# Optimization experiments

Measured on AMD Instinct MI355X. Metric: run time of the kernel, lower is better.

## Reference

```python
import jax, jax.numpy as jnp
import numpy as np

TEMPERATURE = 0.07


def _l2norm(x, axis, eps=1e-12):
    n = jnp.sqrt(jnp.sum(x * x, axis=axis, keepdims=True))
    return x / jnp.maximum(n, eps)


def _bilinear_sample(img, x, y):
    # img: (C,H,W); x,y: (N,) pixel coords. Matches F.grid_sample(mode='bilinear',
    # padding_mode='zeros', align_corners=True) after the norm/denorm round trip.
    C, H, W = img.shape
    x0 = jnp.floor(x); y0 = jnp.floor(y)
    x1 = x0 + 1.0;     y1 = y0 + 1.0
    wx1 = x - x0; wx0 = 1.0 - wx1
    wy1 = y - y0; wy0 = 1.0 - wy1

    def gather(xi, yi, w):
        inb = (xi >= 0) & (xi <= W - 1) & (yi >= 0) & (yi <= H - 1)
        xc = jnp.clip(xi, 0, W - 1).astype(jnp.int32)
        yc = jnp.clip(yi, 0, H - 1).astype(jnp.int32)
        v = img[:, yc, xc]  # (C,N)
        return v * (w * inb)[None, :]

    return (gather(x0, y0, wx0 * wy0) + gather(x1, y0, wx1 * wy0)
            + gather(x0, y1, wx0 * wy1) + gather(x1, y1, wx1 * wy1))


def setup_inputs() -> dict:
    key = jax.random.key(0)
    k1, k2, k3, k4 = jax.random.split(key, 4)
    B, C, Hf, Wf = 32, 256, 64, 64
    Ho, Wo = 512, 512
    fmap_rgb = jax.random.normal(k1, (B, C, Hf, Wf), dtype=jnp.float32)
    fmap_depth = jax.random.normal(k2, (B, C, Hf, Wf), dtype=jnp.float32)
    # uniform coords inside the original image so sampled positions are in-range
    projected_coords = jax.random.uniform(k3, (B, 2, Ho, Wo), dtype=jnp.float32) * (Wo - 1)
    valid_mask = jax.random.uniform(k4, (B, 1, Ho, Wo), dtype=jnp.float32)
    return {"fmap_rgb": fmap_rgb, "fmap_depth": fmap_depth,
            "projected_coords": projected_coords, "valid_mask": valid_mask}


def reference(fmap_rgb, fmap_depth, projected_coords, valid_mask):
    B, C, Hf, Wf = fmap_rgb.shape
    Ho = projected_coords.shape[2]
    ds = Ho // Hf

    fr = _l2norm(fmap_rgb, axis=1)
    fd = _l2norm(fmap_depth, axis=1)

    coords_f = projected_coords[:, :, ::ds, ::ds]   # (B,2,Hf,Wf)
    vm_f = valid_mask[:, :, ::ds, ::ds]             # (B,1,Hf,Wf)

    step = max(1, Hf // 16)
    gh, gw = jnp.meshgrid(jnp.arange(0, Hf, step), jnp.arange(0, Wf, step), indexing='ij')
    ghf = gh.reshape(-1); gwf = gw.reshape(-1)
    N = ghf.shape[0]  # num_grid (~256)

    depth_feats = fd[:, :, ghf, gwf]                # (B,C,N)
    rgb_neg = fr[:, :, ghf, gwf]                    # (B,C,N)
    proj_u = coords_f[:, 0, ghf, gwf] / ds          # (B,N) pixel coords in feat space
    proj_v = coords_f[:, 1, ghf, gwf] / ds
    grid_valid = vm_f[:, 0, ghf, gwf] > 0.5         # (B,N)

    # positive features via bilinear sampling (computed in the original; not used
    # in the loss because labels index into rgb_neg, i.e. the diagonal)
    _rgb_pos = jax.vmap(_bilinear_sample)(fr, proj_u, proj_v)  # (B,C,N)

    sim = jnp.einsum('bcn,bcm->bnm', depth_feats, rgb_neg) / TEMPERATURE  # (B,N,N)

    neg_inf = jnp.asarray(-1e30, sim.dtype)
    sim_m = jnp.where(grid_valid[:, None, :], sim, neg_inf)  # mask invalid columns
    logZ = jax.nn.logsumexp(sim_m, axis=-1)                  # (B,N)
    diag = jnp.einsum('bnn->bn', sim)                        # positive logits
    row_loss = logZ - diag                                   # per-row CE

    vf = grid_valid.astype(sim.dtype)
    n_valid = grid_valid.sum(axis=-1)                        # (B,) int
    include = n_valid >= 2                                   # skip batches with <2 valid
    loss_b = (row_loss * vf).sum(axis=-1) / jnp.maximum(n_valid, 1).astype(sim.dtype)
    avg_loss = jnp.where(include, loss_b, 0.0).sum() / B

    preds = jnp.argmax(sim_m, axis=-1)                       # (B,N)
    correct = (preds == jnp.arange(N)[None, :]) & grid_valid & include[:, None]
    total_count = jnp.where(include, n_valid, 0).sum()
    accuracy = jnp.where(total_count > 0,
                         correct.sum().astype(sim.dtype) /
                         jnp.maximum(total_count, 1).astype(sim.dtype) * 100.0,
                         0.0)
    avg_loss = jnp.where(total_count > 0, avg_loss, 0.0)
    return avg_loss, accuracy
```

## Files before the change

### kernel.cpp

```cpp
#include <hip/hip_runtime.h>
#include <math.h>

#define BB   32
#define CC   256
#define HF   64
#define WF   64
#define NN   256
#define MROWS 32
#define NSTRIP (NN / MROWS)
#define SIMP 260
#define NXCD 8

typedef __attribute__((ext_vector_type(8))) short    bf16x8;
typedef __attribute__((ext_vector_type(4))) float    f32x4;
typedef __attribute__((ext_vector_type(8))) unsigned short u16x8;

__device__ inline unsigned short f2bf(float f) {
    unsigned u = __float_as_uint(f);
    unsigned r = u + 0x7FFFu + ((u >> 16) & 1u);
    return (unsigned short)(r >> 16);
}

__global__ __launch_bounds__(256) void gather_kernel(
        const float* __restrict__ fr,
        const float* __restrict__ fd,
        const float* __restrict__ vm,
        unsigned short* __restrict__ Dbf,
        unsigned short* __restrict__ Rbf,
        float* __restrict__ nPartD,
        float* __restrict__ nPartR,
        float* __restrict__ GV) {
    int blk = blockIdx.x;
    int xcd = blk & (NXCD - 1);
    int r   = blk >> 3;
    int b   = xcd * 4 + (r & 3);
    int cg  = r >> 2;

    int t = threadIdx.x;
    int i = t >> 4, j = t & 15;

    size_t mapBase = (size_t)(b * CC + cg * 16) * (HF * WF);
    size_t ptOff   = (size_t)(4 * i) * WF + 4 * j;

    float ssd = 0.0f, ssr = 0.0f;
    unsigned short dbuf[16], rbuf[16];
#pragma unroll
    for (int cc = 0; cc < 16; ++cc) {
        float vd_ = fd[mapBase + (size_t)cc * (HF * WF) + ptOff];
        float vr_ = fr[mapBase + (size_t)cc * (HF * WF) + ptOff];
        dbuf[cc] = f2bf(vd_);
        rbuf[cc] = f2bf(vr_);
        ssd = fmaf(vd_, vd_, ssd);
        ssr = fmaf(vr_, vr_, ssr);
    }
    unsigned short* dDst = Dbf + ((size_t)(b * NN + t) * CC + cg * 16);
    unsigned short* rDst = Rbf + ((size_t)(b * NN + t) * CC + cg * 16);
    *reinterpret_cast<u16x8*>(dDst)     = *reinterpret_cast<u16x8*>(&dbuf[0]);
    *reinterpret_cast<u16x8*>(dDst + 8) = *reinterpret_cast<u16x8*>(&dbuf[8]);
    *reinterpret_cast<u16x8*>(rDst)     = *reinterpret_cast<u16x8*>(&rbuf[0]);
    *reinterpret_cast<u16x8*>(rDst + 8) = *reinterpret_cast<u16x8*>(&rbuf[8]);

    nPartD[(size_t)(b * 16 + cg) * NN + t] = ssd;
    nPartR[(size_t)(b * 16 + cg) * NN + t] = ssr;

    if (cg == 0) {
        float v = vm[((size_t)b * 512 + 32 * i) * 512 + 32 * j];
        GV[(size_t)b * NN + t] = (v > 0.5f) ? 1.0f : 0.0f;
    }
}

__global__ __launch_bounds__(256) void sim_loss_kernel(
        const unsigned short* __restrict__ Dbf,
        const unsigned short* __restrict__ Rbf,
        const float* __restrict__ nPartD,
        const float* __restrict__ nPartR,
        const float* __restrict__ GV,
        float* __restrict__ lossPart,
        float* __restrict__ corrPart) {
    __shared__ float simLds[MROWS * SIMP];
    __shared__ float colInv[NN];
    __shared__ float validF[NN];
    __shared__ float rowInv[MROWS];
    __shared__ float diagLds[MROWS];
    __shared__ float rowLoss[MROWS];
    __shared__ float rowCorr[MROWS];

    int blk   = blockIdx.x;
    int xcd   = blk & (NXCD - 1);
    int rr    = blk >> 3;
    int b     = xcd * 4 + (rr & 3);
    int strip = rr >> 2;
    int nbase = strip * MROWS;

    int t  = threadIdx.x;
    int w  = t >> 6;
    int l  = t & 63;
    int lg = l >> 4, lr = l & 15;

    {
        float ss = 0.0f;
#pragma unroll
        for (int p = 0; p < 16; ++p) ss += nPartR[(size_t)(b * 16 + p) * NN + t];
        colInv[t] = 1.0f / fmaxf(sqrtf(ss), 1e-12f);
        validF[t] = GV[(size_t)b * NN + t];
    }
    if (t < MROWS) {
        float ss = 0.0f;
#pragma unroll
        for (int p = 0; p < 16; ++p) ss += nPartD[(size_t)(b * 16 + p) * NN + nbase + t];
        rowInv[t] = 1.0f / fmaxf(sqrtf(ss), 1e-12f);
    }
    __syncthreads();

    const unsigned short* Dp = Dbf + (size_t)(b * NN + nbase) * CC;
    const unsigned short* Rp = Rbf + (size_t)b * NN * CC;

    f32x4 acc[2][4] = {};

#pragma unroll
    for (int ks = 0; ks < 8; ++ks) {
        int coff = ks * 32 + lg * 8;
        bf16x8 a0 = *reinterpret_cast<const bf16x8*>(Dp + (size_t)(lr)      * CC + coff);
        bf16x8 a1 = *reinterpret_cast<const bf16x8*>(Dp + (size_t)(16 + lr) * CC + coff);
        bf16x8 b0 = *reinterpret_cast<const bf16x8*>(Rp + (size_t)(w * 64 +  0 + lr) * CC + coff);
        bf16x8 b1 = *reinterpret_cast<const bf16x8*>(Rp + (size_t)(w * 64 + 16 + lr) * CC + coff);
        bf16x8 b2 = *reinterpret_cast<const bf16x8*>(Rp + (size_t)(w * 64 + 32 + lr) * CC + coff);
        bf16x8 b3 = *reinterpret_cast<const bf16x8*>(Rp + (size_t)(w * 64 + 48 + lr) * CC + coff);
        acc[0][0] = __builtin_amdgcn_mfma_f32_16x16x32_bf16(a0, b0, acc[0][0], 0, 0, 0);
        acc[0][1] = __builtin_amdgcn_mfma_f32_16x16x32_bf16(a0, b1, acc[0][1], 0, 0, 0);
        acc[0][2] = __builtin_amdgcn_mfma_f32_16x16x32_bf16(a0, b2, acc[0][2], 0, 0, 0);
        acc[0][3] = __builtin_amdgcn_mfma_f32_16x16x32_bf16(a0, b3, acc[0][3], 0, 0, 0);
        acc[1][0] = __builtin_amdgcn_mfma_f32_16x16x32_bf16(a1, b0, acc[1][0], 0, 0, 0);
        acc[1][1] = __builtin_amdgcn_mfma_f32_16x16x32_bf16(a1, b1, acc[1][1], 0, 0, 0);
        acc[1][2] = __builtin_amdgcn_mfma_f32_16x16x32_bf16(a1, b2, acc[1][2], 0, 0, 0);
        acc[1][3] = __builtin_amdgcn_mfma_f32_16x16x32_bf16(a1, b3, acc[1][3], 0, 0, 0);
    }

    const float invT = 1.0f / 0.07f;
#pragma unroll
    for (int mi = 0; mi < 2; ++mi) {
#pragma unroll
        for (int ni = 0; ni < 4; ++ni) {
            int col = w * 64 + ni * 16 + lr;
            float ci = colInv[col];
            float gv = validF[col];
#pragma unroll
            for (int reg = 0; reg < 4; ++reg) {
                int lrow = mi * 16 + lg * 4 + reg;
                float s = acc[mi][ni][reg] * invT * rowInv[lrow] * ci;
                if (col == nbase + lrow) diagLds[lrow] = s;
                simLds[lrow * SIMP + col] = (gv > 0.5f) ? s : -1e30f;
            }
        }
    }
    __syncthreads();

    for (int k = w; k < MROWS; k += 4) {
        const float* row = &simLds[k * SIMP];
        float v0 = row[l];
        float v1 = row[64 + l];
        float v2 = row[128 + l];
        float v3 = row[192 + l];
        float mv = v0; int mi = l;
        if (v1 > mv) { mv = v1; mi = l + 64; }
        if (v2 > mv) { mv = v2; mi = l + 128; }
        if (v3 > mv) { mv = v3; mi = l + 192; }
#pragma unroll
        for (int off = 32; off > 0; off >>= 1) {
            float ov = __shfl_xor(mv, off, 64);
            int   oi = __shfl_xor(mi, off, 64);
            if (ov > mv || (ov == mv && oi < mi)) { mv = ov; mi = oi; }
        }
        float e = expf(v0 - mv) + expf(v1 - mv) + expf(v2 - mv) + expf(v3 - mv);
#pragma unroll
        for (int off = 32; off > 0; off >>= 1) e += __shfl_xor(e, off, 64);
        if (l == 0) {
            float vfn = validF[nbase + k];
            float lz = mv + logf(e);
            rowLoss[k] = (vfn > 0.5f) ? (lz - diagLds[k]) : 0.0f;
            rowCorr[k] = (vfn > 0.5f && mi == nbase + k) ? 1.0f : 0.0f;
        }
    }
    __syncthreads();

    if (t == 0) {
        float la = 0.0f, ca = 0.0f;
#pragma unroll
        for (int k = 0; k < MROWS; ++k) { la += rowLoss[k]; ca += rowCorr[k]; }
        lossPart[(size_t)b * NSTRIP + strip] = la;
        corrPart[(size_t)b * NSTRIP + strip] = ca;
    }
}

__global__ __launch_bounds__(256) void finalize_kernel(
        const float* __restrict__ GV,
        const float* __restrict__ lossPart,
        const float* __restrict__ corrPart,
        float* __restrict__ out) {
    __shared__ float sl[BB], sc2[BB], st2[BB];
    int t = threadIdx.x;
    int b = t >> 3, s = t & 7;

    float nvp = 0.0f;
    const float4* g4 = reinterpret_cast<const float4*>(GV + (size_t)b * NN);
#pragma unroll
    for (int q = 0; q < 8; ++q) {
        float4 v = g4[s * 8 + q];
        nvp += v.x + v.y + v.z + v.w;
    }
#pragma unroll
    for (int off = 1; off < 8; off <<= 1) nvp += __shfl_xor(nvp, off, 64);

    if (s == 0) {
        float lb = 0.0f, cb = 0.0f;
#pragma unroll
        for (int k = 0; k < NSTRIP; ++k) {
            lb += lossPart[b * NSTRIP + k];
            cb += corrPart[b * NSTRIP + k];
        }
        bool inc = (nvp >= 2.0f);
        sl[b]  = inc ? (lb / fmaxf(nvp, 1.0f)) : 0.0f;
        sc2[b] = inc ? cb : 0.0f;
        st2[b] = inc ? nvp : 0.0f;
    }
    __syncthreads();
    if (t == 0) {
        float L = 0.0f, Ccnt = 0.0f, Tcnt = 0.0f;
        for (int bb = 0; bb < BB; ++bb) { L += sl[bb]; Ccnt += sc2[bb]; Tcnt += st2[bb]; }
        float avg = L / (float)BB;
        out[0] = (Tcnt > 0.0f) ? avg : 0.0f;
        out[1] = (Tcnt > 0.0f) ? (Ccnt / fmaxf(Tcnt, 1.0f) * 100.0f) : 0.0f;
    }
}

extern "C" void kernel_launch(void* const* d_in, const int* in_sizes, int n_in,
                              void* d_out, int out_size, void* d_ws, size_t ws_size,
                              hipStream_t stream) {
    const float* fr = (const float*)d_in[0];
    const float* fd = (const float*)d_in[1];
    const float* vm = (const float*)d_in[3];

    float* out = (float*)d_out;
    char* ws = (char*)d_ws;

    size_t featBytes = (size_t)BB * NN * CC * 2;
    size_t partBytes = (size_t)BB * 16 * NN * 4;
    unsigned short* Dbf = (unsigned short*)ws;
    unsigned short* Rbf = (unsigned short*)(ws + featBytes);
    float* nPartD   = (float*)(ws + 2 * featBytes);
    float* nPartR   = (float*)(ws + 2 * featBytes + partBytes);
    float* GV       = (float*)(ws + 2 * featBytes + 2 * partBytes);
    float* lossPart = GV + (size_t)BB * NN;
    float* corrPart = lossPart + BB * NSTRIP;

    hipLaunchKernelGGL(gather_kernel, dim3(BB * 16), dim3(256), 0, stream,
                       fr, fd, vm, Dbf, Rbf, nPartD, nPartR, GV);
    hipLaunchKernelGGL(sim_loss_kernel, dim3(BB * NSTRIP), dim3(256), 0, stream,
                       Dbf, Rbf, nPartD, nPartR, GV, lossPart, corrPart);
    hipLaunchKernelGGL(finalize_kernel, dim3(1), dim3(256), 0, stream,
                       GV, lossPart, corrPart, out);
}
```

Measured before the change: 38.75 us.

## Fuse finalize into sim kernel via last-block atomic and halve row tiles

Removes the separate finalize kernel launch by having the last sim_loss block (found with an atomic counter) do the global reduction. Row tiles shrink from 32 to 16, which doubles the grid to 512 blocks for better CU coverage. Each block now rereads the full R operand, so global/L2 traffic for R doubles. The change also switches to fast __expf/__logf intrinsics and adds a memset launch to reset the counter.

```diff
diff --git a/kernel.cpp b/kernel.cpp
--- a/kernel.cpp
+++ b/kernel.cpp
@@ -6,10 +6,11 @@
 #define HF   64
 #define WF   64
 #define NN   256
-#define MROWS 32
-#define NSTRIP (NN / MROWS)
+#define TROWS 16
+#define NTILES (NN / TROWS)
 #define SIMP 260
 #define NXCD 8
+#define SIMBLOCKS (BB * NTILES)
 
 typedef __attribute__((ext_vector_type(8))) short    bf16x8;
 typedef __attribute__((ext_vector_type(4))) float    f32x4;
@@ -76,21 +77,24 @@
         const float* __restrict__ nPartR,
         const float* __restrict__ GV,
         float* __restrict__ lossPart,
-        float* __restrict__ corrPart) {
-    __shared__ float simLds[MROWS * SIMP];
+        float* __restrict__ corrPart,
+        unsigned int* __restrict__ doneCnt,
+        float* __restrict__ out) {
+    __shared__ float simLds[TROWS * SIMP];
     __shared__ float colInv[NN];
     __shared__ float validF[NN];
-    __shared__ float rowInv[MROWS];
-    __shared__ float diagLds[MROWS];
-    __shared__ float rowLoss[MROWS];
-    __shared__ float rowCorr[MROWS];
+    __shared__ float rowInv[TROWS];
+    __shared__ float diagLds[TROWS];
+    __shared__ float rowLoss[TROWS];
+    __shared__ float rowCorr[TROWS];
+    __shared__ int   lastFlag;
 
     int blk   = blockIdx.x;
     int xcd   = blk & (NXCD - 1);
     int rr    = blk >> 3;
     int b     = xcd * 4 + (rr & 3);
-    int strip = rr >> 2;
-    int nbase = strip * MROWS;
+    int tile  = rr >> 2;
+    int nbase = tile * TROWS;
 
     int t  = threadIdx.x;
     int w  = t >> 6;
@@ -104,7 +108,7 @@
         colInv[t] = 1.0f / fmaxf(sqrtf(ss), 1e-12f);
         validF[t] = GV[(size_t)b * NN + t];
     }
-    if (t < MROWS) {
+    if (t < TROWS) {
         float ss = 0.0f;
 #pragma unroll
         for (int p = 0; p < 16; ++p) ss += nPartD[(size_t)(b * 16 + p) * NN + nbase + t];
@@ -113,49 +117,41 @@
     __syncthreads();
 
     const unsigned short* Dp = Dbf + (size_t)(b * NN + nbase) * CC;
-    const unsigned short* Rp = Rbf + (size_t)b * NN * CC;
-
-    f32x4 acc[2][4] = {};
-
-#pragma unroll
+    const unsigned short* Rp = Rbf + (size_t)(b * NN + w * 64) * CC;
+
+    f32x4 acc[4] = {};
+
+#pragma unroll 2
     for (int ks = 0; ks < 8; ++ks) {
         int coff = ks * 32 + lg * 8;
-        bf16x8 a0 = *reinterpret_cast<const bf16x8*>(Dp + (size_t)(lr)      * CC + coff);
-        bf16x8 a1 = *reinterpret_cast<const bf16x8*>(Dp + (size_t)(16 + lr) * CC + coff);
-        bf16x8 b0 = *reinterpret_cast<const bf16x8*>(Rp + (size_t)(w * 64 +  0 + lr) * CC + coff);
-        bf16x8 b1 = *reinterpret_cast<const bf16x8*>(Rp + (size_t)(w * 64 + 16 + lr) * CC + coff);
-        bf16x8 b2 = *reinterpret_cast<const bf16x8*>(Rp + (size_t)(w * 64 + 32 + lr) * CC + coff);
-        bf16x8 b3 = *reinterpret_cast<const bf16x8*>(Rp + (size_t)(w * 64 + 48 + lr) * CC + coff);
-        acc[0][0] = __builtin_amdgcn_mfma_f32_16x16x32_bf16(a0, b0, acc[0][0], 0, 0, 0);
-        acc[0][1] = __builtin_amdgcn_mfma_f32_16x16x32_bf16(a0, b1, acc[0][1], 0, 0, 0);
-        acc[0][2] = __builtin_amdgcn_mfma_f32_16x16x32_bf16(a0, b2, acc[0][2], 0, 0, 0);
-        acc[0][3] = __builtin_amdgcn_mfma_f32_16x16x32_bf16(a0, b3, acc[0][3], 0, 0, 0);
-        acc[1][0] = __builtin_amdgcn_mfma_f32_16x16x32_bf16(a1, b0, acc[1][0], 0, 0, 0);
-        acc[1][1] = __builtin_amdgcn_mfma_f32_16x16x32_bf16(a1, b1, acc[1][1], 0, 0, 0);
-        acc[1][2] = __builtin_amdgcn_mfma_f32_16x16x32_bf16(a1, b2, acc[1][2], 0, 0, 0);
-        acc[1][3] = __builtin_amdgcn_mfma_f32_16x16x32_bf16(a1, b3, acc[1][3], 0, 0, 0);
+        bf16x8 a0 = *reinterpret_cast<const bf16x8*>(Dp + (size_t)lr * CC + coff);
+        bf16x8 b0 = *reinterpret_cast<const bf16x8*>(Rp + (size_t)(lr)      * CC + coff);
+        bf16x8 b1 = *reinterpret_cast<const bf16x8*>(Rp + (size_t)(16 + lr) * CC + coff);
+        bf16x8 b2 = *reinterpret_cast<const bf16x8*>(Rp + (size_t)(32 + lr) * CC + coff);
+        bf16x8 b3 = *reinterpret_cast<const bf16x8*>(Rp + (size_t)(48 + lr) * CC + coff);
+        acc[0] = __builtin_amdgcn_mfma_f32_16x16x32_bf16(a0, b0, acc[0], 0, 0, 0);
+        acc[1] = __builtin_amdgcn_mfma_f32_16x16x32_bf16(a0, b1, acc[1], 0, 0, 0);
+        acc[2] = __builtin_amdgcn_mfma_f32_16x16x32_bf16(a0, b2, acc[2], 0, 0, 0);
+        acc[3] = __builtin_amdgcn_mfma_f32_16x16x32_bf16(a0, b3, acc[3], 0, 0, 0);
     }
 
     const float invT = 1.0f / 0.07f;
 #pragma unroll
-    for (int mi = 0; mi < 2; ++mi) {
-#pragma unroll
-        for (int ni = 0; ni < 4; ++ni) {
-            int col = w * 64 + ni * 16 + lr;
-            float ci = colInv[col];
-            float gv = validF[col];
-#pragma unroll
-            for (int reg = 0; reg < 4; ++reg) {
-                int lrow = mi * 16 + lg * 4 + reg;
-                float s = acc[mi][ni][reg] * invT * rowInv[lrow] * ci;
-                if (col == nbase + lrow) diagLds[lrow] = s;
-                simLds[lrow * SIMP + col] = (gv > 0.5f) ? s : -1e30f;
-            }
-        }
-    }
-    __syncthreads();
-
-    for (int k = w; k < MROWS; k += 4) {
+    for (int ni = 0; ni < 4; ++ni) {
+        int col = w * 64 + ni * 16 + lr;
+        float ci = colInv[col];
+        float gv = validF[col];
+#pragma unroll
+        for (int reg = 0; reg < 4; ++reg) {
+            int lrow = lg * 4 + reg;
+            float s = acc[ni][reg] * invT * rowInv[lrow] * ci;
+            if (col == nbase + lrow) diagLds[lrow] = s;
+            simLds[lrow * SIMP + col] = (gv > 0.5f) ? s : -1e30f;
+        }
+    }
+    __syncthreads();
+
+    for (int k = w; k < TROWS; k += 4) {
         const float* row = &simLds[k * SIMP];
         float v0 = row[l];
         float v1 = row[64 + l];
@@ -171,12 +167,12 @@
             int   oi = __shfl_xor(mi, off, 64);
             if (ov > mv || (ov == mv && oi < mi)) { mv = ov; mi = oi; }
         }
-        float e = expf(v0 - mv) + expf(v1 - mv) + expf(v2 - mv) + expf(v3 - mv);
+        float e = __expf(v0 - mv) + __expf(v1 - mv) + __expf(v2 - mv) + __expf(v3 - mv);
 #pragma unroll
         for (int off = 32; off > 0; off >>= 1) e += __shfl_xor(e, off, 64);
         if (l == 0) {
             float vfn = validF[nbase + k];
-            float lz = mv + logf(e);
+            float lz = mv + __logf(e);
             rowLoss[k] = (vfn > 0.5f) ? (lz - diagLds[k]) : 0.0f;
             rowCorr[k] = (vfn > 0.5f && mi == nbase + k) ? 1.0f : 0.0f;
         }
@@ -186,50 +182,50 @@
     if (t == 0) {
         float la = 0.0f, ca = 0.0f;
 #pragma unroll
-        for (int k = 0; k < MROWS; ++k) { la += rowLoss[k]; ca += rowCorr[k]; }
-        lossPart[(size_t)b * NSTRIP + strip] = la;
-        corrPart[(size_t)b * NSTRIP + strip] = ca;
-    }
-}
-
-__global__ __launch_bounds__(256) void finalize_kernel(
-        const float* __restrict__ GV,
-        const float* __restrict__ lossPart,
-        const float* __restrict__ corrPart,
-        float* __restrict__ out) {
-    __shared__ float sl[BB], sc2[BB], st2[BB];
-    int t = threadIdx.x;
-    int b = t >> 3, s = t & 7;
-
-    float nvp = 0.0f;
-    const float4* g4 = reinterpret_cast<const float4*>(GV + (size_t)b * NN);
-#pragma unroll
-    for (int q = 0; q < 8; ++q) {
-        float4 v = g4[s * 8 + q];
-        nvp += v.x + v.y + v.z + v.w;
-    }
-#pragma unroll
-    for (int off = 1; off < 8; off <<= 1) nvp += __shfl_xor(nvp, off, 64);
-
-    if (s == 0) {
-        float lb = 0.0f, cb = 0.0f;
-#pragma unroll
-        for (int k = 0; k < NSTRIP; ++k) {
-            lb += lossPart[b * NSTRIP + k];
-            cb += corrPart[b * NSTRIP + k];
-        }
-        bool inc = (nvp >= 2.0f);
-        sl[b]  = inc ? (lb / fmaxf(nvp, 1.0f)) : 0.0f;
-        sc2[b] = inc ? cb : 0.0f;
-        st2[b] = inc ? nvp : 0.0f;
-    }
-    __syncthreads();
-    if (t == 0) {
-        float L = 0.0f, Ccnt = 0.0f, Tcnt = 0.0f;
-        for (int bb = 0; bb < BB; ++bb) { L += sl[bb]; Ccnt += sc2[bb]; Tcnt += st2[bb]; }
-        float avg = L / (float)BB;
-        out[0] = (Tcnt > 0.0f) ? avg : 0.0f;
-        out[1] = (Tcnt > 0.0f) ? (Ccnt / fmaxf(Tcnt, 1.0f) * 100.0f) : 0.0f;
+        for (int k = 0; k < TROWS; ++k) { la += rowLoss[k]; ca += rowCorr[k]; }
+        lossPart[(size_t)b * NTILES + tile] = la;
+        corrPart[(size_t)b * NTILES + tile] = ca;
+        __threadfence();
+        unsigned old = atomicAdd(doneCnt, 1u);
+        lastFlag = (old == SIMBLOCKS - 1) ? 1 : 0;
+    }
+    __syncthreads();
+
+    if (lastFlag) {
+        __threadfence();
+        __shared__ float sl[BB], sc2[BB], st2[BB];
+        int bb = t >> 3, s = t & 7;
+
+        float nvp = 0.0f;
+        const float4* g4 = reinterpret_cast<const float4*>(GV + (size_t)bb * NN);
+#pragma unroll
+        for (int q = 0; q < 8; ++q) {
+            float4 v = g4[s * 8 + q];
+            nvp += v.x + v.y + v.z + v.w;
+        }
+#pragma unroll
+        for (int off = 1; off < 8; off <<= 1) nvp += __shfl_xor(nvp, off, 64);
+
+        if (s == 0) {
+            float lb = 0.0f, cb = 0.0f;
+#pragma unroll
+            for (int k = 0; k < NTILES; ++k) {
+                lb += lossPart[bb * NTILES + k];
+                cb += corrPart[bb * NTILES + k];
+            }
+            bool inc = (nvp >= 2.0f);
+            sl[bb]  = inc ? (lb / fmaxf(nvp, 1.0f)) : 0.0f;
+            sc2[bb] = inc ? cb : 0.0f;
+            st2[bb] = inc ? nvp : 0.0f;
+        }
+        __syncthreads();
+        if (t == 0) {
+            float L = 0.0f, Ccnt = 0.0f, Tcnt = 0.0f;
+            for (int q = 0; q < BB; ++q) { L += sl[q]; Ccnt += sc2[q]; Tcnt += st2[q]; }
+            float avg = L / (float)BB;
+            out[0] = (Tcnt > 0.0f) ? avg : 0.0f;
+            out[1] = (Tcnt > 0.0f) ? (Ccnt / fmaxf(Tcnt, 1.0f) * 100.0f) : 0.0f;
+        }
     }
 }
 
@@ -251,12 +247,14 @@
     float* nPartR   = (float*)(ws + 2 * featBytes + partBytes);
     float* GV       = (float*)(ws + 2 * featBytes + 2 * partBytes);
     float* lossPart = GV + (size_t)BB * NN;
-    float* corrPart = lossPart + BB * NSTRIP;
+    float* corrPart = lossPart + BB * NTILES;
+    unsigned int* doneCnt = (unsigned int*)(corrPart + BB * NTILES);
+
+    hipMemsetAsync(doneCnt, 0, sizeof(unsigned int), stream);
 
     hipLaunchKernelGGL(gather_kernel, dim3(BB * 16), dim3(256), 0, stream,
                        fr, fd, vm, Dbf, Rbf, nPartD, nPartR, GV);
-    hipLaunchKernelGGL(sim_loss_kernel, dim3(BB * NSTRIP), dim3(256), 0, stream,
-                       Dbf, Rbf, nPartD, nPartR, GV, lossPart, corrPart);
-    hipLaunchKernelGGL(finalize_kernel, dim3(1), dim3(256), 0, stream,
-                       GV, lossPart, corrPart, out);
-}
+    hipLaunchKernelGGL(sim_loss_kernel, dim3(SIMBLOCKS), dim3(256), 0, stream,
+                       Dbf, Rbf, nPartD, nPartR, GV, lossPart, corrPart,
+                       doneCnt, out);
+}
```

Result: slower. 53.84 us (+39.0%).
